# Optimization experiments

Hardware: AMD Instinct MI355X
Metric: run time of the kernel (lower is better)

## Reference

```python
import jax, jax.numpy as jnp
import numpy as np

RADIUS = 0.4
K = 32
EPS = 1e-5


def ball_query(xyz, new_xyz, radius, k):
    """xyz: (B,N,3), new_xyz: (B,M,3) -> idx (B,M,k) int32.
    Replicates CUDA ball_query: first k points within radius (in index order),
    padded with the first found index."""
    N = xyz.shape[1]
    # squared distances (B,M,N)
    d2 = jnp.sum((new_xyz[:, :, None, :] - xyz[:, None, :, :]) ** 2, axis=-1)
    within = d2 < radius * radius
    order = jnp.arange(N, dtype=jnp.int32)
    key = jnp.where(within, order[None, None, :], N)
    idx_sorted = jnp.argsort(key, axis=-1)[..., :k].astype(jnp.int32)  # (B,M,k)
    cnt = within.sum(axis=-1)  # (B,M)
    first = idx_sorted[..., :1]
    slot = jnp.arange(k)[None, None, :]
    return jnp.where(slot < cnt[..., None], idx_sorted, first)


def gather_bmk(x_bnc, idx):
    """x_bnc: (B,N,C), idx: (B,M,K) -> (B,M,K,C)"""
    return jnp.take_along_axis(x_bnc[:, None, :, :], idx[..., None], axis=2)


def conv_bn_relu(x, w, b, gamma, beta):
    """x: (B,Cin,M,K); w: (Cout,Cin). 1x1 Conv2d + BatchNorm2d (train stats) + ReLU."""
    x = jnp.einsum('bcmk,oc->bomk', x, w) + b[None, :, None, None]
    mu = x.mean(axis=(0, 2, 3), keepdims=True)
    var = x.var(axis=(0, 2, 3), keepdims=True)
    x = gamma[None, :, None, None] * (x - mu) * jax.lax.rsqrt(var + EPS) + beta[None, :, None, None]
    return jax.nn.relu(x)


def setup_inputs() -> dict:
    key = jax.random.key(0)
    ks = jax.random.split(key, 16)
    B, N, C, M = 4, 16384, 128, 1024
    mlp = [131, 128, 128, 256]
    inp = {
        'points_xyz': jax.random.normal(ks[0], (B, N, 3), dtype=jnp.float32),
        'features': jax.random.normal(ks[1], (B, C, N), dtype=jnp.float32),
        'indices': jax.random.randint(ks[2], (B, M), 0, N, dtype=jnp.int32),
    }
    for i in range(3):
        cin, cout = mlp[i], mlp[i + 1]
        inp[f'w{i+1}'] = jax.random.normal(ks[3 + 4 * i], (cout, cin), dtype=jnp.float32) / np.sqrt(cin)
        inp[f'b{i+1}'] = jnp.zeros((cout,), dtype=jnp.float32)
        inp[f'g{i+1}'] = jnp.ones((cout,), dtype=jnp.float32)
        inp[f'beta{i+1}'] = jnp.zeros((cout,), dtype=jnp.float32)
    return inp


def reference(points_xyz, features, indices,
              w1, b1, g1, beta1, w2, b2, g2, beta2, w3, b3, g3, beta3):
    # sample centers: new_xyz (B,M,3)
    new_xyz = jnp.take_along_axis(points_xyz, indices[..., None], axis=1)
    # ball query + group
    idx = ball_query(points_xyz, new_xyz, RADIUS, K)            # (B,M,K)
    grouped_xyz = gather_bmk(points_xyz, idx) - new_xyz[:, :, None, :]  # (B,M,K,3)
    grouped_feat = gather_bmk(features.transpose(0, 2, 1), idx)         # (B,M,K,C)
    x = jnp.concatenate([grouped_xyz, grouped_feat], axis=-1)           # (B,M,K,3+C)
    x = x.transpose(0, 3, 1, 2)                                         # (B,3+C,M,K)
    # shared MLP (1x1 Conv2d + BN + ReLU)
    x = conv_bn_relu(x, w1, b1, g1, beta1)
    x = conv_bn_relu(x, w2, b2, g2, beta2)
    x = conv_bn_relu(x, w3, b3, g3, beta3)
    # max pool over K -> (B, Cout, M)
    new_features = x.max(axis=-1)
    return new_xyz, new_features
```

## Files before the change

### kernel.cpp

```cpp
#include <hip/hip_runtime.h>

#define B_ 4
#define N_ 16384
#define C_ 128
#define M_ 1024
#define K_ 32
#define NTOT (B_*M_*K_)
#define RAD2 0.16f
#define EPS_ 1e-5f

typedef unsigned short ushort_t;
typedef __bf16 bf16x8 __attribute__((ext_vector_type(8)));
typedef float f32x4 __attribute__((ext_vector_type(4)));

__device__ __forceinline__ float b2f(ushort_t u){
  unsigned int x = ((unsigned int)u) << 16;
  return __builtin_bit_cast(float, x);
}
__device__ __forceinline__ ushort_t f2b(float f){
  unsigned int u = __builtin_bit_cast(unsigned int, f);
  unsigned int r = (u + 0x7FFFu + ((u >> 16) & 1u)) >> 16;
  return (ushort_t)r;
}

__device__ __forceinline__ void ball_query_part(
    int bi, const float* __restrict__ xyz, const int* __restrict__ indices,
    float* __restrict__ new_xyz, int* __restrict__ idx)
{
  int t = threadIdx.x;
  int wv = t >> 6, lane = t & 63;
  int g = bi*4 + wv;
  int b = g >> 10;
  const float* pb = xyz + (size_t)b*N_*3;
  const float4* pb4 = (const float4*)pb;
  int qi = indices[g];
  float qx = pb[qi*3+0], qy = pb[qi*3+1], qz = pb[qi*3+2];
  if (lane < 3) new_xyz[g*3 + lane] = pb[qi*3 + lane];

  int cnt = 0, firstIdx = 0;
  int* op = idx + g*K_;

  float4 buf0[6], buf1[6];
  #pragma unroll
  for (int i = 0; i < 6; i++) buf0[i] = pb4[lane*6 + i];

  auto process = [&](const float4* buf, int chunk){
    const float* f = (const float*)buf;
    unsigned int local_mask = 0;
    #pragma unroll
    for (int j = 0; j < 8; j++){
      float dx = f[j*3+0]-qx, dy = f[j*3+1]-qy, dz = f[j*3+2]-qz;
      if (dx*dx + dy*dy + dz*dz < RAD2) local_mask |= (1u << j);
    }
    if (__ballot(local_mask != 0) == 0ull) return;
    int base = chunk*512;
    int lcnt = __popc(local_mask);
    int incl = lcnt;
    #pragma unroll
    for (int d = 1; d < 64; d <<= 1){
      int tt = __shfl_up(incl, d);
      if (lane >= d) incl += tt;
    }
    int excl = incl - lcnt;
    int total = __shfl(incl, 63);
    if (cnt == 0){
      int lf = local_mask ? (lane*8 + __builtin_ctz(local_mask)) : 0x7fffffff;
      #pragma unroll
      for (int d = 1; d < 64; d <<= 1) lf = min(lf, __shfl_xor(lf, d));
      firstIdx = base + lf;
    }
    int sl = cnt + excl;
    unsigned int m = local_mask;
    while (m && sl < K_){
      int j = __builtin_ctz(m); m &= m - 1u;
      op[sl++] = base + lane*8 + j;
    }
    cnt += total;
  };

  for (int chunk = 0; chunk < 32; chunk += 2){
    if (chunk + 1 < 32){
      #pragma unroll
      for (int i = 0; i < 6; i++) buf1[i] = pb4[(chunk+1)*384 + lane*6 + i];
    }
    process(buf0, chunk);
    if (cnt >= K_) break;
    if (chunk + 2 < 32){
      #pragma unroll
      for (int i = 0; i < 6; i++) buf0[i] = pb4[(chunk+2)*384 + lane*6 + i];
    }
    process(buf1, chunk + 1);
    if (cnt >= K_) break;
  }
  if (cnt < K_){
    for (int s = cnt + lane; s < K_; s += 64) op[s] = firstIdx;
  }
}

__global__ __launch_bounds__(256) void setup_k(
    const float* __restrict__ xyz, const float* __restrict__ feat,
    const int* __restrict__ indices,
    const float* __restrict__ w1, const float* __restrict__ w2, const float* __restrict__ w3,
    float* __restrict__ new_xyz, int* __restrict__ idx,
    ushort_t* __restrict__ ftr_t,
    ushort_t* __restrict__ W1b, ushort_t* __restrict__ W2b, ushort_t* __restrict__ W3b)
{
  __shared__ float T[32][133];
  int blk = blockIdx.x;
  int t = threadIdx.x;
  if (blk < 1024){
    ball_query_part(blk, xyz, indices, new_xyz, idx);
  } else if (blk < 3072){
    int bi = blk - 1024;
    int b = bi >> 9, ntile = bi & 511;
    int n0 = ntile * 32;
    int nl = t & 31;
    #pragma unroll
    for (int ci = 0; ci < 16; ci++){
      int c = ci*8 + (t >> 5);
      T[nl][c] = feat[((size_t)b*C_ + c)*N_ + n0 + nl];
    }
    __syncthreads();
    #pragma unroll
    for (int ii = 0; ii < 2; ii++){
      int v = ii*256 + t;
      int n2 = v >> 4, seg = v & 15;
      union { ushort_t u[8]; uint4 q; } pk;
      #pragma unroll
      for (int j = 0; j < 8; j++) pk.u[j] = f2b(T[n2][seg*8 + j]);
      *(uint4*)(ftr_t + ((size_t)b*N_ + n0 + n2)*C_ + seg*8) = pk.q;
    }
  } else {
    const int T1 = 128*160, T2 = 128*128, T3 = 256*128;
    for (int e = (blk - 3072)*256 + t; e < T1+T2+T3; e += 64*256){
      if (e < T1){
        int o = e / 160, c = e % 160;
        float v = 0.f;
        if (c < 128) v = w1[o*131 + 3 + c];
        else if (c < 131) v = w1[o*131 + (c - 128)];
        W1b[e] = f2b(v);
      } else if (e < T1+T2){
        int e2 = e - T1;
        W2b[e2] = f2b(w2[e2]);
      } else {
        int e3 = e - T1 - T2;
        W3b[e3] = f2b(w3[e3]);
      }
    }
  }
}

__global__ __launch_bounds__(256, 2) void conv1_k(
    const float* __restrict__ xyz, const ushort_t* __restrict__ ftr_t,
    const int* __restrict__ idx, const float* __restrict__ new_xyz,
    const ushort_t* __restrict__ W1b, const float* __restrict__ b1,
    ushort_t* __restrict__ Y1, float* __restrict__ sumO, float* __restrict__ sqO)
{
  __shared__ alignas(16) ushort_t Xs[32*168];
  __shared__ alignas(16) float Ys[32*68];
  int t = threadIdx.x;
  int wv = t >> 6, lane = t & 63, quad = lane >> 4, l15 = lane & 15;
  int row = t >> 3, chunk = t & 7;
  int col0 = (blockIdx.x & 1) * 64;
  int blk = blockIdx.x >> 1;

  if (t < 128){
    int rr = t >> 2, cc = t & 3;
    *(uint4*)(Xs + rr*168 + 128 + cc*8) = make_uint4(0,0,0,0);
  }
  bf16x8 wf[5];
  #pragma unroll
  for (int kt = 0; kt < 5; kt++)
    wf[kt] = *(const bf16x8*)(W1b + (col0 + wv*16 + l15)*160 + kt*32 + quad*8);
  float bs_r = b1[col0 + wv*16 + l15];
  float s = 0.f, s2 = 0.f;

  const int GPB = 4;
  int g0 = blk * GPB;
  int b = g0 >> 10;
  int ia[GPB], ibv[GPB];
  #pragma unroll
  for (int i = 0; i < GPB; i++){
    ia[i]  = idx[(g0+i)*K_ + row];
    ibv[i] = idx[(g0+i)*K_ + (t & 31)];
  }
  for (int i = 0; i < GPB; i++){
    int g = g0 + i;
    const ushort_t* src = ftr_t + ((size_t)b*N_ + ia[i])*C_ + chunk*16;
    uint4 q0 = *(const uint4*)src;
    uint4 q1 = *(const uint4*)(src + 8);
    *(uint4*)(Xs + row*168 + chunk*16) = q0;
    *(uint4*)(Xs + row*168 + chunk*16 + 8) = q1;
    if (t < 32){
      const float* pp = xyz + ((size_t)b*N_ + ibv[i])*3;
      const float* qq = new_xyz + (size_t)g*3;
      unsigned int u0 = (unsigned int)f2b(pp[0]-qq[0]) | ((unsigned int)f2b(pp[1]-qq[1]) << 16);
      unsigned int u1 = (unsigned int)f2b(pp[2]-qq[2]);
      *(uint2*)(Xs + t*168 + 128) = make_uint2(u0, u1);
    }
    __syncthreads();
    bf16x8 af[2][5];
    #pragma unroll
    for (int mt = 0; mt < 2; mt++)
      #pragma unroll
      for (int kt = 0; kt < 5; kt++)
        af[mt][kt] = *(const bf16x8*)(Xs + (mt*16 + l15)*168 + kt*32 + quad*8);
    f32x4 acc[2] = {(f32x4){0,0,0,0}, (f32x4){0,0,0,0}};
    #pragma unroll
    for (int kt = 0; kt < 5; kt++){
      acc[0] = __builtin_amdgcn_mfma_f32_16x16x32_bf16(af[0][kt], wf[kt], acc[0], 0,0,0);
      acc[1] = __builtin_amdgcn_mfma_f32_16x16x32_bf16(af[1][kt], wf[kt], acc[1], 0,0,0);
    }
    {
      int o = wv*16 + l15;
      #pragma unroll
      for (int mt = 0; mt < 2; mt++)
        #pragma unroll
        for (int r = 0; r < 4; r++){
          float v = acc[mt][r] + bs_r;
          s += v; s2 += v*v;
          Ys[(mt*16 + quad*4 + r)*68 + o] = v;
        }
    }
    __syncthreads();
    {
      const float* yp = &Ys[row*68 + chunk*8];
      f32x4 y0 = *(const f32x4*)(yp);
      f32x4 y1 = *(const f32x4*)(yp + 4);
      union { ushort_t u[8]; uint4 q; } p0;
      #pragma unroll
      for (int j = 0; j < 4; j++){
        p0.u[j] = f2b(y0[j]); p0.u[4+j] = f2b(y1[j]);
      }
      *(uint4*)(Y1 + ((size_t)g*K_ + row)*128 + col0 + chunk*8) = p0.q;
    }
  }
  s  += __shfl_xor(s, 16);  s  += __shfl_xor(s, 32);
  s2 += __shfl_xor(s2, 16); s2 += __shfl_xor(s2, 32);
  if (quad == 0){
    int o = col0 + wv*16 + l15;
    atomicAdd(&sumO[o], s);
    atomicAdd(&sqO[o], s2);
  }
}

template<int COUT, bool MAXMIN>
__global__ __launch_bounds__(256, 2) void convB_k(
    const ushort_t* __restrict__ Yin, const ushort_t* __restrict__ Wb,
    const float* __restrict__ bias, const float* __restrict__ g_bn,
    const float* __restrict__ beta_bn, const float* __restrict__ sumI,
    const float* __restrict__ sqI, ushort_t* __restrict__ Yout,
    unsigned int* __restrict__ Ymm, float* __restrict__ sumO, float* __restrict__ sqO)
{
  constexpr int HALF = COUT/2;
  constexpr int NT = HALF/64;
  constexpr int NXS = MAXMIN ? 2 : 1;
  __shared__ alignas(16) ushort_t Xs[NXS][32*136];
  __shared__ alignas(16) float Ys[MAXMIN ? 4 : 32*68];
  int t = threadIdx.x;
  int wv = t >> 6, lane = t & 63, quad = lane >> 4, l15 = lane & 15;
  int row = t >> 3, chunk = t & 7;
  int col0 = (blockIdx.x & 1) * HALF;
  int blk = blockIdx.x >> 1;

  float a_r[16], d_r[16];
  #pragma unroll
  for (int j = 0; j < 16; j++){
    int c = chunk*16 + j;
    float mu  = sumI[c] * (1.f/NTOT);
    float var = sqI[c]  * (1.f/NTOT) - mu*mu;
    float a = g_bn[c] * rsqrtf(var + EPS_);
    a_r[j] = a; d_r[j] = beta_bn[c] - a*mu;
  }
  bf16x8 wf[NT][4];
  #pragma unroll
  for (int nt = 0; nt < NT; nt++)
    #pragma unroll
    for (int kt = 0; kt < 4; kt++)
      wf[nt][kt] = *(const bf16x8*)(Wb + (col0 + wv*(NT*16) + nt*16 + l15)*128 + kt*32 + quad*8);
  float bs_r[NT];
  #pragma unroll
  for (int nt = 0; nt < NT; nt++) bs_r[nt] = bias[col0 + wv*(NT*16) + nt*16 + l15];
  float s[NT], s2[NT];
  #pragma unroll
  for (int nt = 0; nt < NT; nt++){ s[nt] = 0.f; s2[nt] = 0.f; }

  const int GPB = 4;
  int g0 = blk * GPB;
  uint4 r0, r1;
  {
    const ushort_t* src = Yin + ((size_t)g0*K_ + row)*128 + chunk*16;
    r0 = *(const uint4*)src; r1 = *(const uint4*)(src + 8);
  }
  for (int i = 0; i < GPB; i++){
    int g = g0 + i;
    ushort_t* X = Xs[MAXMIN ? (i & (NXS-1)) : 0];
    union { ushort_t u[8]; uint4 q; } i0, i1, o0, o1;
    i0.q = r0; i1.q = r1;
    #pragma unroll
    for (int j = 0; j < 8; j++){
      o0.u[j] = f2b(fmaxf(a_r[j]  *b2f(i0.u[j]) + d_r[j],   0.f));
      o1.u[j] = f2b(fmaxf(a_r[8+j]*b2f(i1.u[j]) + d_r[8+j], 0.f));
    }
    *(uint4*)(X + row*136 + chunk*16) = o0.q;
    *(uint4*)(X + row*136 + chunk*16 + 8) = o1.q;
    if (i + 1 < GPB){
      const ushort_t* src = Yin + ((size_t)(g+1)*K_ + row)*128 + chunk*16;
      r0 = *(const uint4*)src; r1 = *(const uint4*)(src + 8);
    }
    __syncthreads();
    bf16x8 af[2][4];
    #pragma unroll
    for (int mt = 0; mt < 2; mt++)
      #pragma unroll
      for (int kt = 0; kt < 4; kt++)
        af[mt][kt] = *(const bf16x8*)(X + (mt*16 + l15)*136 + kt*32 + quad*8);
    f32x4 acc[NT][2];
    #pragma unroll
    for (int nt = 0; nt < NT; nt++){ acc[nt][0] = (f32x4){0,0,0,0}; acc[nt][1] = (f32x4){0,0,0,0}; }
    #pragma unroll
    for (int nt = 0; nt < NT; nt++)
      #pragma unroll
      for (int kt = 0; kt < 4; kt++){
        acc[nt][0] = __builtin_amdgcn_mfma_f32_16x16x32_bf16(af[0][kt], wf[nt][kt], acc[nt][0], 0,0,0);
        acc[nt][1] = __builtin_amdgcn_mfma_f32_16x16x32_bf16(af[1][kt], wf[nt][kt], acc[nt][1], 0,0,0);
      }
    if constexpr (!MAXMIN){
      {
        int o = wv*16 + l15;
        #pragma unroll
        for (int mt = 0; mt < 2; mt++)
          #pragma unroll
          for (int r = 0; r < 4; r++){
            float v = acc[0][mt][r] + bs_r[0];
            s[0] += v; s2[0] += v*v;
            Ys[(mt*16 + quad*4 + r)*68 + o] = v;
          }
      }
      __syncthreads();
      const float* yp = &Ys[row*68 + chunk*8];
      f32x4 y0 = *(const f32x4*)(yp);
      f32x4 y1 = *(const f32x4*)(yp + 4);
      union { ushort_t u[8]; uint4 q; } p0;
      #pragma unroll
      for (int j = 0; j < 4; j++){
        p0.u[j] = f2b(y0[j]); p0.u[4+j] = f2b(y1[j]);
      }
      *(uint4*)(Yout + ((size_t)g*K_ + row)*128 + col0 + chunk*8) = p0.q;
    } else {
      #pragma unroll
      for (int nt = 0; nt < NT; nt++){
        float v0 = acc[nt][0][0] + bs_r[nt];
        float mx = v0, mn = v0;
        s[nt] += v0; s2[nt] += v0*v0;
        #pragma unroll
        for (int mt = 0; mt < 2; mt++)
          #pragma unroll
          for (int r = 0; r < 4; r++){
            if (mt == 0 && r == 0) continue;
            float v = acc[nt][mt][r] + bs_r[nt];
            s[nt] += v; s2[nt] += v*v;
            mx = fmaxf(mx, v); mn = fminf(mn, v);
          }
        mx = fmaxf(mx, __shfl_xor(mx, 16)); mx = fmaxf(mx, __shfl_xor(mx, 32));
        mn = fminf(mn, __shfl_xor(mn, 16)); mn = fminf(mn, __shfl_xor(mn, 32));
        if (quad == 0){
          int o = col0 + wv*(NT*16) + nt*16 + l15;
          Ymm[(size_t)g*256 + o] = (unsigned int)f2b(mx) | ((unsigned int)f2b(mn) << 16);
        }
      }
    }
  }
  #pragma unroll
  for (int nt = 0; nt < NT; nt++){
    s[nt]  += __shfl_xor(s[nt], 16);  s[nt]  += __shfl_xor(s[nt], 32);
    s2[nt] += __shfl_xor(s2[nt], 16); s2[nt] += __shfl_xor(s2[nt], 32);
    if (quad == 0){
      int o = col0 + wv*(NT*16) + nt*16 + l15;
      atomicAdd(&sumO[o], s[nt]);
      atomicAdd(&sqO[o], s2[nt]);
    }
  }
}

__global__ __launch_bounds__(256) void finalize_k(
    const unsigned int* __restrict__ Ymm, const float* __restrict__ g3,
    const float* __restrict__ beta3, const float* __restrict__ sum3,
    const float* __restrict__ sq3, float* __restrict__ out)
{
  __shared__ float T[16][264];
  __shared__ float abn[256], dbn[256];
  int t = threadIdx.x;
  int b = blockIdx.x >> 6;
  int m0 = (blockIdx.x & 63) * 16;
  {
    float mu  = sum3[t] * (1.f/NTOT);
    float var = sq3[t]  * (1.f/NTOT) - mu*mu;
    float a = g3[t] * rsqrtf(var + EPS_);
    abn[t] = a; dbn[t] = beta3[t] - a*mu;
  }
  __syncthreads();
  #pragma unroll
  for (int i = 0; i < 4; i++){
    int v4 = i*256 + t;
    int m = v4 >> 6, oq = (v4 & 63) * 4;
    uint4 w = *(const uint4*)(Ymm + ((size_t)(b*M_ + m0 + m))*256 + oq);
    unsigned int wsv[4] = {w.x, w.y, w.z, w.w};
    float r[4];
    #pragma unroll
    for (int j = 0; j < 4; j++){
      int o = oq + j;
      float mx = b2f((ushort_t)(wsv[j] & 0xffffu));
      float mn = b2f((ushort_t)(wsv[j] >> 16));
      float a = abn[o];
      float val = (a >= 0.f) ? (a*mx + dbn[o]) : (a*mn + dbn[o]);
      r[j] = fmaxf(val, 0.f);
    }
    *(f32x4*)(&T[m][oq]) = *(f32x4*)r;
  }
  __syncthreads();
  #pragma unroll
  for (int p = 0; p < 4; p++){
    int o = p*64 + (t >> 2), c = t & 3;
    float4 v = make_float4(T[c*4+0][o], T[c*4+1][o], T[c*4+2][o], T[c*4+3][o]);
    *(float4*)(out + ((size_t)(b*256 + o))*M_ + m0 + c*4) = v;
  }
}

extern "C" void kernel_launch(void* const* d_in, const int* in_sizes, int n_in,
                              void* d_out, int out_size, void* d_ws, size_t ws_size,
                              hipStream_t stream)
{
  (void)in_sizes; (void)n_in; (void)out_size; (void)ws_size;
  const float* xyz  = (const float*)d_in[0];
  const float* feat = (const float*)d_in[1];
  const int*   inds = (const int*)d_in[2];
  const float* w1 = (const float*)d_in[3];
  const float* b1 = (const float*)d_in[4];
  const float* g1 = (const float*)d_in[5];
  const float* be1= (const float*)d_in[6];
  const float* w2 = (const float*)d_in[7];
  const float* b2 = (const float*)d_in[8];
  const float* g2 = (const float*)d_in[9];
  const float* be2= (const float*)d_in[10];
  const float* w3 = (const float*)d_in[11];
  const float* b3 = (const float*)d_in[12];
  const float* g3 = (const float*)d_in[13];
  const float* be3= (const float*)d_in[14];

  char* ws = (char*)d_ws;
  float* stats = (float*)ws;
  float* s1sum = stats + 0*256;  float* s1sq = stats + 1*256;
  float* s2sum = stats + 2*256;  float* s2sq = stats + 3*256;
  float* s3sum = stats + 4*256;  float* s3sq = stats + 5*256;
  size_t off = 6*256*sizeof(float);
  int* idx = (int*)(ws + off);                off += (size_t)B_*M_*K_*4;
  ushort_t* ftr_t = (ushort_t*)(ws + off);    off += (size_t)B_*N_*C_*2;
  ushort_t* W1b = (ushort_t*)(ws + off);      off += 128*160*2;
  ushort_t* W2b = (ushort_t*)(ws + off);      off += 128*128*2;
  ushort_t* W3b = (ushort_t*)(ws + off);      off += 256*128*2;
  ushort_t* Y1 = (ushort_t*)(ws + off);       off += (size_t)NTOT*128*2;
  ushort_t* Y2 = (ushort_t*)(ws + off);       off += (size_t)NTOT*128*2;
  unsigned int* Ymm = (unsigned int*)(ws + off); off += (size_t)B_*M_*256*4;

  float* new_xyz  = (float*)d_out;
  float* out_feat = (float*)d_out + (size_t)B_*M_*3;

  hipMemsetAsync(stats, 0, 6*256*sizeof(float), stream);
  setup_k<<<3136, 256, 0, stream>>>(xyz, feat, inds, w1, w2, w3,
                                    new_xyz, idx, ftr_t, W1b, W2b, W3b);
  conv1_k<<<2048, 256, 0, stream>>>(xyz, ftr_t, idx, new_xyz, W1b, b1, Y1, s1sum, s1sq);
  convB_k<128,false><<<2048, 256, 0, stream>>>(Y1, W2b, b2, g1, be1, s1sum, s1sq, Y2, nullptr, s2sum, s2sq);
  convB_k<256,true ><<<2048, 256, 0, stream>>>(Y2, W3b, b3, g2, be2, s2sum, s2sq, nullptr, Ymm, s3sum, s3sq);
  finalize_k<<<256, 256, 0, stream>>>(Ymm, g3, be3, s3sum, s3sq, out_feat);
}
```

Before: 243.8 us.

## Give each wave full output columns in conv3 and double groups per block

Conv1 and conv2 now process 8 groups per block instead of 4, with half the grid, which halves the number of times each block loads its weights and flushes its stats. Conv3 is rewritten so each wave owns a private LDS tile and a 64-column slice of the 256 outputs, covering all columns for 4 groups per block. This removes the block-level barriers and the reading of each input tile by two separate blocks (one per column half). The cost is more per-wave input loading and BN work, plus a larger LDS footprint in conv3 that may reduce occupancy.

```diff
diff --git a/kernel.cpp b/kernel.cpp
--- a/kernel.cpp
+++ b/kernel.cpp
@@ -175,7 +175,7 @@
   float bs_r = b1[col0 + wv*16 + l15];
   float s = 0.f, s2 = 0.f;
 
-  const int GPB = 4;
+  const int GPB = 8;
   int g0 = blk * GPB;
   int b = g0 >> 10;
   int ia[GPB], ibv[GPB];
@@ -244,23 +244,19 @@
   }
 }
 
-template<int COUT, bool MAXMIN>
-__global__ __launch_bounds__(256, 2) void convB_k(
+__global__ __launch_bounds__(256, 2) void conv2_k(
     const ushort_t* __restrict__ Yin, const ushort_t* __restrict__ Wb,
     const float* __restrict__ bias, const float* __restrict__ g_bn,
     const float* __restrict__ beta_bn, const float* __restrict__ sumI,
     const float* __restrict__ sqI, ushort_t* __restrict__ Yout,
-    unsigned int* __restrict__ Ymm, float* __restrict__ sumO, float* __restrict__ sqO)
-{
-  constexpr int HALF = COUT/2;
-  constexpr int NT = HALF/64;
-  constexpr int NXS = MAXMIN ? 2 : 1;
-  __shared__ alignas(16) ushort_t Xs[NXS][32*136];
-  __shared__ alignas(16) float Ys[MAXMIN ? 4 : 32*68];
+    float* __restrict__ sumO, float* __restrict__ sqO)
+{
+  __shared__ alignas(16) ushort_t Xs[32*136];
+  __shared__ alignas(16) float Ys[32*68];
   int t = threadIdx.x;
   int wv = t >> 6, lane = t & 63, quad = lane >> 4, l15 = lane & 15;
   int row = t >> 3, chunk = t & 7;
-  int col0 = (blockIdx.x & 1) * HALF;
+  int col0 = (blockIdx.x & 1) * 64;
   int blk = blockIdx.x >> 1;
 
   float a_r[16], d_r[16];
@@ -272,20 +268,14 @@
     float a = g_bn[c] * rsqrtf(var + EPS_);
     a_r[j] = a; d_r[j] = beta_bn[c] - a*mu;
   }
-  bf16x8 wf[NT][4];
-  #pragma unroll
-  for (int nt = 0; nt < NT; nt++)
-    #pragma unroll
-    for (int kt = 0; kt < 4; kt++)
-      wf[nt][kt] = *(const bf16x8*)(Wb + (col0 + wv*(NT*16) + nt*16 + l15)*128 + kt*32 + quad*8);
-  float bs_r[NT];
-  #pragma unroll
-  for (int nt = 0; nt < NT; nt++) bs_r[nt] = bias[col0 + wv*(NT*16) + nt*16 + l15];
-  float s[NT], s2[NT];
-  #pragma unroll
-  for (int nt = 0; nt < NT; nt++){ s[nt] = 0.f; s2[nt] = 0.f; }
-
-  const int GPB = 4;
+  bf16x8 wf[4];
+  #pragma unroll
+  for (int kt = 0; kt < 4; kt++)
+    wf[kt] = *(const bf16x8*)(Wb + (col0 + wv*16 + l15)*128 + kt*32 + quad*8);
+  float bs_r = bias[col0 + wv*16 + l15];
+  float s = 0.f, s2 = 0.f;
+
+  const int GPB = 8;
   int g0 = blk * GPB;
   uint4 r0, r1;
   {
@@ -294,7 +284,6 @@
   }
   for (int i = 0; i < GPB; i++){
     int g = g0 + i;
-    ushort_t* X = Xs[MAXMIN ? (i & (NXS-1)) : 0];
     union { ushort_t u[8]; uint4 q; } i0, i1, o0, o1;
     i0.q = r0; i1.q = r1;
     #pragma unroll
@@ -302,8 +291,8 @@
       o0.u[j] = f2b(fmaxf(a_r[j]  *b2f(i0.u[j]) + d_r[j],   0.f));
       o1.u[j] = f2b(fmaxf(a_r[8+j]*b2f(i1.u[j]) + d_r[8+j], 0.f));
     }
-    *(uint4*)(X + row*136 + chunk*16) = o0.q;
-    *(uint4*)(X + row*136 + chunk*16 + 8) = o1.q;
+    *(uint4*)(Xs + row*136 + chunk*16) = o0.q;
+    *(uint4*)(Xs + row*136 + chunk*16 + 8) = o1.q;
     if (i + 1 < GPB){
       const ushort_t* src = Yin + ((size_t)(g+1)*K_ + row)*128 + chunk*16;
       r0 = *(const uint4*)src; r1 = *(const uint4*)(src + 8);
@@ -314,69 +303,142 @@
     for (int mt = 0; mt < 2; mt++)
       #pragma unroll
       for (int kt = 0; kt < 4; kt++)
+        af[mt][kt] = *(const bf16x8*)(Xs + (mt*16 + l15)*136 + kt*32 + quad*8);
+    f32x4 acc[2] = {(f32x4){0,0,0,0}, (f32x4){0,0,0,0}};
+    #pragma unroll
+    for (int kt = 0; kt < 4; kt++){
+      acc[0] = __builtin_amdgcn_mfma_f32_16x16x32_bf16(af[0][kt], wf[kt], acc[0], 0,0,0);
+      acc[1] = __builtin_amdgcn_mfma_f32_16x16x32_bf16(af[1][kt], wf[kt], acc[1], 0,0,0);
+    }
+    {
+      int o = wv*16 + l15;
+      #pragma unroll
+      for (int mt = 0; mt < 2; mt++)
+        #pragma unroll
+        for (int r = 0; r < 4; r++){
+          float v = acc[mt][r] + bs_r;
+          s += v; s2 += v*v;
+          Ys[(mt*16 + quad*4 + r)*68 + o] = v;
+        }
+    }
+    __syncthreads();
+    {
+      const float* yp = &Ys[row*68 + chunk*8];
+      f32x4 y0 = *(const f32x4*)(yp);
+      f32x4 y1 = *(const f32x4*)(yp + 4);
+      union { ushort_t u[8]; uint4 q; } p0;
+      #pragma unroll
+      for (int j = 0; j < 4; j++){
+        p0.u[j] = f2b(y0[j]); p0.u[4+j] = f2b(y1[j]);
+      }
+      *(uint4*)(Yout + ((size_t)g*K_ + row)*128 + col0 + chunk*8) = p0.q;
+    }
+  }
+  s  += __shfl_xor(s, 16);  s  += __shfl_xor(s, 32);
+  s2 += __shfl_xor(s2, 16); s2 += __shfl_xor(s2, 32);
+  if (quad == 0){
+    int o = col0 + wv*16 + l15;
+    atomicAdd(&sumO[o], s);
+    atomicAdd(&sqO[o], s2);
+  }
+}
+
+__global__ __launch_bounds__(256, 2) void conv3_k(
+    const ushort_t* __restrict__ Yin, const ushort_t* __restrict__ Wb,
+    const float* __restrict__ bias, const float* __restrict__ g_bn,
+    const float* __restrict__ beta_bn, const float* __restrict__ sumI,
+    const float* __restrict__ sqI, unsigned int* __restrict__ Ymm,
+    float* __restrict__ sumO, float* __restrict__ sqO)
+{
+  __shared__ alignas(16) ushort_t Xs[4][32*136];
+  int t = threadIdx.x;
+  int wv = t >> 6, lane = t & 63, quad = lane >> 4, l15 = lane & 15;
+  int rq = lane >> 3, cchunk = lane & 7;
+  ushort_t* X = Xs[wv];
+  int col0w = wv * 64;
+
+  float a_r[16], d_r[16];
+  #pragma unroll
+  for (int j = 0; j < 16; j++){
+    int c = cchunk*16 + j;
+    float mu  = sumI[c] * (1.f/NTOT);
+    float var = sqI[c]  * (1.f/NTOT) - mu*mu;
+    float a = g_bn[c] * rsqrtf(var + EPS_);
+    a_r[j] = a; d_r[j] = beta_bn[c] - a*mu;
+  }
+  bf16x8 wf[4][4];
+  #pragma unroll
+  for (int nt = 0; nt < 4; nt++)
+    #pragma unroll
+    for (int kt = 0; kt < 4; kt++)
+      wf[nt][kt] = *(const bf16x8*)(Wb + (col0w + nt*16 + l15)*128 + kt*32 + quad*8);
+  float bs_r[4];
+  #pragma unroll
+  for (int nt = 0; nt < 4; nt++) bs_r[nt] = bias[col0w + nt*16 + l15];
+  float s[4] = {0,0,0,0}, s2[4] = {0,0,0,0};
+
+  const int GPW = 4;
+  int g0 = blockIdx.x * GPW;
+  for (int i = 0; i < GPW; i++){
+    int g = g0 + i;
+    const ushort_t* src = Yin + ((size_t)g*K_ + rq*4)*128 + cchunk*16;
+    #pragma unroll
+    for (int rr = 0; rr < 4; rr++){
+      union { ushort_t u[8]; uint4 q; } i0, i1, o0, o1;
+      i0.q = *(const uint4*)(src + rr*128);
+      i1.q = *(const uint4*)(src + rr*128 + 8);
+      #pragma unroll
+      for (int j = 0; j < 8; j++){
+        o0.u[j] = f2b(fmaxf(a_r[j]  *b2f(i0.u[j]) + d_r[j],   0.f));
+        o1.u[j] = f2b(fmaxf(a_r[8+j]*b2f(i1.u[j]) + d_r[8+j], 0.f));
+      }
+      *(uint4*)(X + (rq*4+rr)*136 + cchunk*16) = o0.q;
+      *(uint4*)(X + (rq*4+rr)*136 + cchunk*16 + 8) = o1.q;
+    }
+    bf16x8 af[2][4];
+    #pragma unroll
+    for (int mt = 0; mt < 2; mt++)
+      #pragma unroll
+      for (int kt = 0; kt < 4; kt++)
         af[mt][kt] = *(const bf16x8*)(X + (mt*16 + l15)*136 + kt*32 + quad*8);
-    f32x4 acc[NT][2];
-    #pragma unroll
-    for (int nt = 0; nt < NT; nt++){ acc[nt][0] = (f32x4){0,0,0,0}; acc[nt][1] = (f32x4){0,0,0,0}; }
-    #pragma unroll
-    for (int nt = 0; nt < NT; nt++)
+    f32x4 acc[4][2];
+    #pragma unroll
+    for (int nt = 0; nt < 4; nt++){ acc[nt][0] = (f32x4){0,0,0,0}; acc[nt][1] = (f32x4){0,0,0,0}; }
+    #pragma unroll
+    for (int nt = 0; nt < 4; nt++)
       #pragma unroll
       for (int kt = 0; kt < 4; kt++){
         acc[nt][0] = __builtin_amdgcn_mfma_f32_16x16x32_bf16(af[0][kt], wf[nt][kt], acc[nt][0], 0,0,0);
         acc[nt][1] = __builtin_amdgcn_mfma_f32_16x16x32_bf16(af[1][kt], wf[nt][kt], acc[nt][1], 0,0,0);
       }
-    if constexpr (!MAXMIN){
-      {
-        int o = wv*16 + l15;
+    #pragma unroll
+    for (int nt = 0; nt < 4; nt++){
+      float v0 = acc[nt][0][0] + bs_r[nt];
+      float mx = v0, mn = v0;
+      s[nt] += v0; s2[nt] += v0*v0;
+      #pragma unroll
+      for (int mt = 0; mt < 2; mt++)
         #pragma unroll
-        for (int mt = 0; mt < 2; mt++)
-          #pragma unroll
-          for (int r = 0; r < 4; r++){
-            float v = acc[0][mt][r] + bs_r[0];
-            s[0] += v; s2[0] += v*v;
-            Ys[(mt*16 + quad*4 + r)*68 + o] = v;
-          }
+        for (int r = 0; r < 4; r++){
+          if (mt == 0 && r == 0) continue;
+          float v = acc[nt][mt][r] + bs_r[nt];
+          s[nt] += v; s2[nt] += v*v;
+          mx = fmaxf(mx, v); mn = fminf(mn, v);
+        }
+      mx = fmaxf(mx, __shfl_xor(mx, 16)); mx = fmaxf(mx, __shfl_xor(mx, 32));
+      mn = fminf(mn, __shfl_xor(mn, 16)); mn = fminf(mn, __shfl_xor(mn, 32));
+      if (quad == 0){
+        Ymm[(size_t)g*256 + col0w + nt*16 + l15] =
+            (unsigned int)f2b(mx) | ((unsigned int)f2b(mn) << 16);
       }
-      __syncthreads();
-      const float* yp = &Ys[row*68 + chunk*8];
-      f32x4 y0 = *(const f32x4*)(yp);
-      f32x4 y1 = *(const f32x4*)(yp + 4);
-      union { ushort_t u[8]; uint4 q; } p0;
-      #pragma unroll
-      for (int j = 0; j < 4; j++){
-        p0.u[j] = f2b(y0[j]); p0.u[4+j] = f2b(y1[j]);
-      }
-      *(uint4*)(Yout + ((size_t)g*K_ + row)*128 + col0 + chunk*8) = p0.q;
-    } else {
-      #pragma unroll
-      for (int nt = 0; nt < NT; nt++){
-        float v0 = acc[nt][0][0] + bs_r[nt];
-        float mx = v0, mn = v0;
-        s[nt] += v0; s2[nt] += v0*v0;
-        #pragma unroll
-        for (int mt = 0; mt < 2; mt++)
-          #pragma unroll
-          for (int r = 0; r < 4; r++){
-            if (mt == 0 && r == 0) continue;
-            float v = acc[nt][mt][r] + bs_r[nt];
-            s[nt] += v; s2[nt] += v*v;
-            mx = fmaxf(mx, v); mn = fminf(mn, v);
-          }
-        mx = fmaxf(mx, __shfl_xor(mx, 16)); mx = fmaxf(mx, __shfl_xor(mx, 32));
-        mn = fminf(mn, __shfl_xor(mn, 16)); mn = fminf(mn, __shfl_xor(mn, 32));
-        if (quad == 0){
-          int o = col0 + wv*(NT*16) + nt*16 + l15;
-          Ymm[(size_t)g*256 + o] = (unsigned int)f2b(mx) | ((unsigned int)f2b(mn) << 16);
-        }
-      }
-    }
-  }
-  #pragma unroll
-  for (int nt = 0; nt < NT; nt++){
+    }
+  }
+  #pragma unroll
+  for (int nt = 0; nt < 4; nt++){
     s[nt]  += __shfl_xor(s[nt], 16);  s[nt]  += __shfl_xor(s[nt], 32);
     s2[nt] += __shfl_xor(s2[nt], 16); s2[nt] += __shfl_xor(s2[nt], 32);
     if (quad == 0){
-      int o = col0 + wv*(NT*16) + nt*16 + l15;
+      int o = col0w + nt*16 + l15;
       atomicAdd(&sumO[o], s[nt]);
       atomicAdd(&sqO[o], s2[nt]);
     }
@@ -469,8 +531,8 @@
   hipMemsetAsync(stats, 0, 6*256*sizeof(float), stream);
   setup_k<<<3136, 256, 0, stream>>>(xyz, feat, inds, w1, w2, w3,
                                     new_xyz, idx, ftr_t, W1b, W2b, W3b);
-  conv1_k<<<2048, 256, 0, stream>>>(xyz, ftr_t, idx, new_xyz, W1b, b1, Y1, s1sum, s1sq);
-  convB_k<128,false><<<2048, 256, 0, stream>>>(Y1, W2b, b2, g1, be1, s1sum, s1sq, Y2, nullptr, s2sum, s2sq);
-  convB_k<256,true ><<<2048, 256, 0, stream>>>(Y2, W3b, b3, g2, be2, s2sum, s2sq, nullptr, Ymm, s3sum, s3sq);
+  conv1_k<<<1024, 256, 0, stream>>>(xyz, ftr_t, idx, new_xyz, W1b, b1, Y1, s1sum, s1sq);
+  conv2_k<<<1024, 256, 0, stream>>>(Y1, W2b, b2, g1, be1, s1sum, s1sq, Y2, s2sum, s2sq);
+  conv3_k<<<1024, 256, 0, stream>>>(Y2, W3b, b3, g2, be2, s2sum, s2sq, Ymm, s3sum, s3sq);
   finalize_k<<<256, 256, 0, stream>>>(Ymm, g3, be3, s3sum, s3sq, out_feat);
 }
```

Result: faster. 236.1 us (-3.2%).
